# Kernel tuning notes

Hardware: AMD Instinct MI355X
Metric: run time of the kernel (lower is better)

## Reference

```python
import jax, jax.numpy as jnp
import numpy as np

B, T, D = 8, 2048, 1024
GAMMA = 0.96875


def setup_inputs() -> dict:
    key = jax.random.key(0)
    ks = jax.random.split(key, 7)
    sD = 1.0 / np.sqrt(D)
    sT = 1.0 / np.sqrt(T)
    return {
        "x": jax.random.normal(ks[0], (B, T, D), dtype=jnp.float32),
        "Wq": jax.random.normal(ks[1], (D, D), dtype=jnp.float32) * sD,
        "Wk": jax.random.normal(ks[2], (D, D), dtype=jnp.float32) * sD,
        "Wv": jax.random.normal(ks[3], (D, D), dtype=jnp.float32) * sD,
        "W_ih": jax.random.normal(ks[4], (T, T), dtype=jnp.float32) * sT,
        "W_hh": jax.random.normal(ks[5], (T, T), dtype=jnp.float32) * sT,
        "b_ih": jax.random.normal(ks[6], (T,), dtype=jnp.float32) * sT,
    }


def reference(x, Wq, Wk, Wv, W_ih, W_hh, b_ih):
    # x: [B, T, D]; QKV projections (Linear with no bias: x @ W^T)
    Q = jnp.einsum("btd,ed->bte", x, Wq)
    K = jnp.einsum("btd,ed->bte", x, Wk)
    V = jnp.einsum("btd,ed->bte", x, Wv)

    # retention state injected as hidden bias of the tanh-RNN: [B, T]
    bias = jnp.sum(K * V, axis=-1)

    gamma = jnp.full((T,), GAMMA, dtype=x.dtype)
    u = gamma @ W_ih.T + b_ih  # input contribution, identical every step: [T]

    def step(h, b_t):
        h_new = jnp.tanh(u + h @ W_hh.T + b_t)
        return h_new, h_new

    h0 = jnp.zeros((T,), dtype=x.dtype)
    _, S = jax.lax.scan(step, h0, bias)  # scan over the B rows -> S: [B, T]

    # vmap(mul)(S, Q^T)^T  ==  out[b,t,d] = S[b,t] * Q[b,t,d]
    return S[:, :, None] * Q
```

## Files before the change

### kernel.cpp

```cpp
#include <hip/hip_runtime.h>
#include <stdint.h>

#define T_DIM 2048
#define D_DIM 1024
#define B_DIM 8
#define M_TOK (B_DIM * T_DIM)
#define GAMMA_C 0.96875f

typedef float f32x4 __attribute__((ext_vector_type(4)));
typedef float f32x16 __attribute__((ext_vector_type(16)));
typedef float fl4 __attribute__((ext_vector_type(4)));
typedef __bf16 bf16x8 __attribute__((ext_vector_type(8)));
typedef unsigned short us8 __attribute__((ext_vector_type(8)));
typedef unsigned short us4 __attribute__((ext_vector_type(4)));

__device__ __forceinline__ unsigned short f32_bf16_rne(float f) {
  uint32_t u = __builtin_bit_cast(uint32_t, f);
  return (unsigned short)((u + 0x7FFFu + ((u >> 16) & 1u)) >> 16);
}
__device__ __forceinline__ float bf16_f32(unsigned short h) {
  uint32_t u = ((uint32_t)h) << 16;
  return __builtin_bit_cast(float, u);
}

__device__ __forceinline__ int swz_row(int r) {
  return ((r >> 1) & 3) ^ ((r >> 3) & 3);
}

__device__ __forceinline__ void gload16(const void* g, void* l) {
  __builtin_amdgcn_global_load_lds(
      reinterpret_cast<const __attribute__((address_space(1))) uint32_t*>(
          reinterpret_cast<uintptr_t>(g)),
      reinterpret_cast<__attribute__((address_space(3))) uint32_t*>(
          reinterpret_cast<uintptr_t>(l)),
      16, 0, 0);
}

__device__ __forceinline__ bf16x8 ldfrag(const unsigned short* p) {
  us8 u = *reinterpret_cast<const us8*>(p);
  return __builtin_bit_cast(bf16x8, u);
}

#define VMW(n) asm volatile("s_waitcnt vmcnt(" #n ")" ::: "memory")
#define BAR    __builtin_amdgcn_s_barrier()

__global__ __launch_bounds__(256) void k_split(const float* __restrict__ in, int n8,
                                               unsigned short* __restrict__ hi,
                                               unsigned short* __restrict__ lo) {
  int stride = gridDim.x * blockDim.x;
  for (int i = blockIdx.x * blockDim.x + threadIdx.x; i < n8; i += stride) {
    fl4 v0 = ((const fl4*)in)[i * 2];
    fl4 v1 = ((const fl4*)in)[i * 2 + 1];
    us8 h, l;
#pragma unroll
    for (int j = 0; j < 4; ++j) {
      unsigned short hb = f32_bf16_rne(v0[j]);
      h[j] = hb;
      l[j] = f32_bf16_rne(v0[j] - bf16_f32(hb));
      unsigned short hb1 = f32_bf16_rne(v1[j]);
      h[j + 4] = hb1;
      l[j + 4] = f32_bf16_rne(v1[j] - bf16_f32(hb1));
    }
    ((us8*)hi)[i] = h;
    ((us8*)lo)[i] = l;
  }
}

__global__ __launch_bounds__(256) void k_split_hi(const float* __restrict__ in, int n8,
                                                  unsigned short* __restrict__ hi) {
  int stride = gridDim.x * blockDim.x;
  for (int i = blockIdx.x * blockDim.x + threadIdx.x; i < n8; i += stride) {
    fl4 v0 = ((const fl4*)in)[i * 2];
    fl4 v1 = ((const fl4*)in)[i * 2 + 1];
    us8 h;
#pragma unroll
    for (int j = 0; j < 4; ++j) {
      h[j] = f32_bf16_rne(v0[j]);
      h[j + 4] = f32_bf16_rne(v1[j]);
    }
    ((us8*)hi)[i] = h;
  }
}

__global__ __launch_bounds__(256) void k_split_T(const float* __restrict__ in,
                                                 unsigned short* __restrict__ th,
                                                 unsigned short* __restrict__ tl) {
  __shared__ float tile[64][69];
  int be = blockIdx.x >> 4, bd = blockIdx.x & 15;
  int e0 = be * 64, d0 = bd * 64;
  int r = threadIdx.x >> 4;
  int c = (threadIdx.x & 15) * 4;
#pragma unroll
  for (int it = 0; it < 4; ++it) {
    int rr = r + it * 16;
    fl4 v = *(const fl4*)(in + (size_t)(e0 + rr) * D_DIM + d0 + c);
#pragma unroll
    for (int j = 0; j < 4; ++j) tile[rr][c + j] = v[j];
  }
  __syncthreads();
#pragma unroll
  for (int it = 0; it < 4; ++it) {
    int dr = r + it * 16;
    us4 h, l;
#pragma unroll
    for (int j = 0; j < 4; ++j) {
      float f = tile[c + j][dr];
      h[j] = f32_bf16_rne(f);
      l[j] = f32_bf16_rne(f - bf16_f32(h[j]));
    }
    *(us4*)(th + (size_t)(d0 + dr) * D_DIM + e0 + c) = h;
    *(us4*)(tl + (size_t)(d0 + dr) * D_DIM + e0 + c) = l;
  }
}

__global__ __launch_bounds__(256) void k_u(const float* __restrict__ Wih,
                                           const float* __restrict__ bih,
                                           float* __restrict__ u) {
  int wave = threadIdx.x >> 6, lane = threadIdx.x & 63;
  int t = blockIdx.x * 4 + wave;
  const fl4* row = (const fl4*)(Wih + (size_t)t * T_DIM);
  float s = 0.f;
#pragma unroll
  for (int i = 0; i < 8; ++i) {
    fl4 v = row[lane + i * 64];
    s += v[0] + v[1] + v[2] + v[3];
  }
#pragma unroll
  for (int m = 32; m >= 1; m >>= 1) s += __shfl_xor(s, m, 64);
  if (lane == 0) u[t] = GAMMA_C * s + bih[t];
}

__global__ __launch_bounds__(256) void k_step_bf(const unsigned short* __restrict__ Whh_b,
                                                 const float* __restrict__ hprev,
                                                 const float* __restrict__ u,
                                                 const float* __restrict__ biasrow,
                                                 float* __restrict__ hout) {
  int wave = threadIdx.x >> 6, lane = threadIdx.x & 63;
  int t = blockIdx.x * 4 + wave;
  const unsigned short* row = Whh_b + (size_t)t * T_DIM;
  float s = 0.f;
#pragma unroll
  for (int i = 0; i < 4; ++i) {
    us8 w = *(const us8*)(row + i * 512 + lane * 8);
    fl4 h0 = *(const fl4*)(hprev + i * 512 + lane * 8);
    fl4 h1 = *(const fl4*)(hprev + i * 512 + lane * 8 + 4);
    s += bf16_f32(w[0]) * h0[0] + bf16_f32(w[1]) * h0[1] +
         bf16_f32(w[2]) * h0[2] + bf16_f32(w[3]) * h0[3] +
         bf16_f32(w[4]) * h1[0] + bf16_f32(w[5]) * h1[1] +
         bf16_f32(w[6]) * h1[2] + bf16_f32(w[7]) * h1[3];
  }
#pragma unroll
  for (int m = 32; m >= 1; m >>= 1) s += __shfl_xor(s, m, 64);
  if (lane == 0) hout[t] = tanhf(u[t] + s + biasrow[t]);
}

__global__ __launch_bounds__(256) void k_ht(
    const unsigned short* __restrict__ ah, const unsigned short* __restrict__ al,
    const unsigned short* __restrict__ bh, const unsigned short* __restrict__ bl,
    float* __restrict__ Hf) {
  __shared__ unsigned short sAh[2][64 * 32], sAl[2][64 * 32];
  __shared__ unsigned short sBh[2][64 * 32], sBl[2][64 * 32];
  const int tid = threadIdx.x;
  const int wave = tid >> 6, lane = tid & 63;
  const int wm = wave >> 1, wn = wave & 1;
  const int m0 = (blockIdx.x >> 4) * 64, n0 = (blockIdx.x & 15) * 64;
  const int hi32 = lane >> 5;

  const int srow = tid >> 2;
  const int csrc = (tid & 3) ^ swz_row(srow);
  const size_t ga = (size_t)(m0 + srow) * D_DIM + csrc * 8;
  const size_t gb = (size_t)(n0 + srow) * D_DIM + csrc * 8;
  const int ldst = tid * 8;

  f32x16 acc = {};
  const int l31 = lane & 31;
  const int sw = swz_row(l31);
  const int ar = wm * 32 + l31;
  const int br = wn * 32 + l31;
  int aoff[2], boff[2];
#pragma unroll
  for (int kh = 0; kh < 2; ++kh) {
    aoff[kh] = ar * 32 + (((kh * 2 + hi32) ^ sw) * 8);
    boff[kh] = br * 32 + (((kh * 2 + hi32) ^ sw) * 8);
  }

  auto stage = [&](int t, int buf) {
    const size_t ko = (size_t)t * 32;
    gload16(ah + ga + ko, &sAh[buf][ldst]);
    gload16(al + ga + ko, &sAl[buf][ldst]);
    gload16(bh + gb + ko, &sBh[buf][ldst]);
    gload16(bl + gb + ko, &sBl[buf][ldst]);
  };

  stage(0, 0);
  stage(1, 1);
  for (int kt = 0; kt < 32; ++kt) {
    const int cur = kt & 1;
    if (kt < 31) { VMW(4); } else { VMW(0); }
    BAR;
#pragma unroll
    for (int kh = 0; kh < 2; ++kh) {
      bf16x8 fah = ldfrag(&sAh[cur][aoff[kh]]);
      bf16x8 fal = ldfrag(&sAl[cur][aoff[kh]]);
      bf16x8 fbh = ldfrag(&sBh[cur][boff[kh]]);
      bf16x8 fbl = ldfrag(&sBl[cur][boff[kh]]);
      acc = __builtin_amdgcn_mfma_f32_32x32x16_bf16(fah, fbh, acc, 0, 0, 0);
      acc = __builtin_amdgcn_mfma_f32_32x32x16_bf16(fah, fbl, acc, 0, 0, 0);
      acc = __builtin_amdgcn_mfma_f32_32x32x16_bf16(fal, fbh, acc, 0, 0, 0);
    }
    BAR;
    if (kt + 2 <= 31) stage(kt + 2, cur);
  }
#pragma unroll
  for (int r = 0; r < 16; ++r) {
    int row = m0 + wm * 32 + (r & 3) + 8 * (r >> 2) + 4 * hi32;
    int col = n0 + wn * 32 + l31;
    Hf[(size_t)row * D_DIM + col] = acc[r];
  }
}

__global__ __launch_bounds__(256) void k_nprime(const float* __restrict__ Hf,
                                                unsigned short* __restrict__ mh,
                                                unsigned short* __restrict__ ml) {
  __shared__ float t2[64][65];
  const int ti = blockIdx.x >> 4;
  const int tj = blockIdx.x & 15;
  const int r0 = ti * 64, c0 = tj * 64;
  const int a = threadIdx.x >> 2;
  const int b4 = (threadIdx.x & 3) * 16;
  if (tj < ti) {
#pragma unroll
    for (int j = 0; j < 16; ++j) {
      size_t ad = (size_t)(r0 + a) * D_DIM + c0 + b4 + j;
      mh[ad] = 0;
      ml[ad] = 0;
    }
    return;
  }
#pragma unroll
  for (int j = 0; j < 16; j += 4) {
    fl4 v = *(const fl4*)(Hf + (size_t)(c0 + a) * D_DIM + r0 + b4 + j);
#pragma unroll
    for (int q = 0; q < 4; ++q) t2[a][b4 + j + q] = v[q];
  }
  __syncthreads();
#pragma unroll
  for (int j = 0; j < 16; ++j) {
    int dp = r0 + a;
    int dd = c0 + b4 + j;
    float v = 0.f;
    if (dd > dp)       v = Hf[(size_t)dp * D_DIM + dd] + t2[b4 + j][a];
    else if (dd == dp) v = Hf[(size_t)dp * D_DIM + dd];
    unsigned short hb = f32_bf16_rne(v);
    unsigned short lb = f32_bf16_rne(v - bf16_f32(hb));
    size_t ad = (size_t)dp * D_DIM + dd;
    mh[ad] = hb;
    ml[ad] = lb;
  }
}

__global__ __launch_bounds__(256, 4) void k_y_bias(
    const unsigned short* __restrict__ xh, const unsigned short* __restrict__ xl,
    const unsigned short* __restrict__ bh, const unsigned short* __restrict__ bl,
    float* __restrict__ bias) {
  __shared__ unsigned short sAh[2][128 * 16], sAl[2][128 * 16];
  __shared__ unsigned short sBh[2][128 * 16], sBl[2][128 * 16];
  const int tid = threadIdx.x;
  const int wave = tid >> 6, lane = tid & 63;
  const int wm = wave >> 1, wn = wave & 1;
  const int xcd = blockIdx.x & 7, seq = blockIdx.x >> 3;
  const int mb = xcd * 16 + (seq >> 2);
  const int np = seq & 3;
  const int m0 = mb * 128;
  const int hi32 = lane >> 5;
  const int l31 = lane & 31;

  const int srow = tid >> 1;
  const int cch = tid & 1;
  const size_t gA = (size_t)(m0 + srow) * D_DIM + cch * 8;
  const int ldst = tid * 8;

  int aoff[2], boff[2];
#pragma unroll
  for (int mi = 0; mi < 2; ++mi)
    aoff[mi] = (wm * 64 + mi * 32 + l31) * 16 + hi32 * 8;
#pragma unroll
  for (int ni = 0; ni < 2; ++ni)
    boff[ni] = (wn * 64 + ni * 32 + l31) * 16 + hi32 * 8;

  auto phase = [&](int nb) {
    const int n0 = nb * 128;
    const int k0 = nb * 8;
    const int ke = 64;
    const size_t gB = (size_t)(n0 + srow) * D_DIM + cch * 8;

    auto stage = [&](int t, int buf) {
      const size_t ko = (size_t)t * 16;
      gload16(xh + gA + ko, &sAh[buf][ldst]);
      gload16(xl + gA + ko, &sAl[buf][ldst]);
      gload16(bh + gB + ko, &sBh[buf][ldst]);
      gload16(bl + gB + ko, &sBl[buf][ldst]);
    };

    f32x16 acc[2][2] = {};
    stage(k0, 0);
    stage(k0 + 1, 1);
    for (int kt = k0; kt < ke; ++kt) {
      const int cur = (kt - k0) & 1;
      if (kt < ke - 1) { VMW(4); } else { VMW(0); }
      BAR;
      {
        bf16x8 fah[2], fal[2], fbh_[2], fbl_[2];
#pragma unroll
        for (int mi = 0; mi < 2; ++mi) {
          fah[mi] = ldfrag(&sAh[cur][aoff[mi]]);
          fal[mi] = ldfrag(&sAl[cur][aoff[mi]]);
        }
#pragma unroll
        for (int ni = 0; ni < 2; ++ni) {
          fbh_[ni] = ldfrag(&sBh[cur][boff[ni]]);
          fbl_[ni] = ldfrag(&sBl[cur][boff[ni]]);
        }
        __builtin_amdgcn_s_setprio(1);
#pragma unroll
        for (int mi = 0; mi < 2; ++mi)
#pragma unroll
          for (int ni = 0; ni < 2; ++ni) {
            acc[mi][ni] = __builtin_amdgcn_mfma_f32_32x32x16_bf16(fah[mi], fbh_[ni], acc[mi][ni], 0, 0, 0);
            acc[mi][ni] = __builtin_amdgcn_mfma_f32_32x32x16_bf16(fah[mi], fbl_[ni], acc[mi][ni], 0, 0, 0);
            acc[mi][ni] = __builtin_amdgcn_mfma_f32_32x32x16_bf16(fal[mi], fbh_[ni], acc[mi][ni], 0, 0, 0);
          }
        __builtin_amdgcn_s_setprio(0);
      }
      BAR;
      if (kt + 2 < ke) stage(kt + 2, cur);
    }

#pragma unroll
    for (int mi = 0; mi < 2; ++mi)
#pragma unroll
      for (int r = 0; r < 16; ++r) {
        int row = m0 + wm * 64 + mi * 32 + (r & 3) + 8 * (r >> 2) + 4 * hi32;
        size_t ix = (size_t)row * D_DIM + n0 + wn * 64 + l31;
        float xv0 = bf16_f32(xh[ix]) + bf16_f32(xl[ix]);
        float xv1 = bf16_f32(xh[ix + 32]) + bf16_f32(xl[ix + 32]);
        float p = xv0 * acc[mi][0][r] + xv1 * acc[mi][1][r];
        p += __shfl_xor(p, 1, 64);
        p += __shfl_xor(p, 2, 64);
        p += __shfl_xor(p, 4, 64);
        p += __shfl_xor(p, 8, 64);
        p += __shfl_xor(p, 16, 64);
        if (l31 == 0) atomicAdd(&bias[row], p);
      }
  };

  phase(np);
  phase(7 - np);
}

__global__ __launch_bounds__(256, 4) void k_q_out(
    const unsigned short* __restrict__ xh,
    const unsigned short* __restrict__ qh_,
    const float* __restrict__ S, float* __restrict__ out) {
  __shared__ unsigned short sA[2][128 * 32];
  __shared__ unsigned short sB[2][128 * 32];
  const int tid = threadIdx.x;
  const int wave = tid >> 6, lane = tid & 63;
  const int wm = wave >> 1, wn = wave & 1;
  int sw0 = (blockIdx.x & 7) * 128 + (blockIdx.x >> 3);
  const int mb = sw0 >> 3, nb = sw0 & 7;
  const int m0 = mb * 128, n0 = nb * 128;
  const int hi32 = lane >> 5;
  const int l31 = lane & 31;

  const int srow0 = tid >> 2, srow1 = srow0 + 64;
  const int csrc0 = (tid & 3) ^ swz_row(srow0);
  const int csrc1 = (tid & 3) ^ swz_row(srow1);
  const size_t gaA0 = (size_t)(m0 + srow0) * D_DIM + csrc0 * 8;
  const size_t gaA1 = (size_t)(m0 + srow1) * D_DIM + csrc1 * 8;
  const size_t gaB0 = (size_t)(n0 + srow0) * D_DIM + csrc0 * 8;
  const size_t gaB1 = (size_t)(n0 + srow1) * D_DIM + csrc1 * 8;
  const int ldst0 = tid * 8, ldst1 = (tid + 256) * 8;

  f32x16 acc[2][2] = {};
  int aoff[2][2], boff[2][2];
#pragma unroll
  for (int mi = 0; mi < 2; ++mi) {
    int r = wm * 64 + mi * 32 + l31;
    int sw = swz_row(r);
#pragma unroll
    for (int kh = 0; kh < 2; ++kh)
      aoff[mi][kh] = r * 32 + (((kh * 2 + hi32) ^ sw) * 8);
  }
#pragma unroll
  for (int ni = 0; ni < 2; ++ni) {
    int r = wn * 64 + ni * 32 + l31;
    int sw = swz_row(r);
#pragma unroll
    for (int kh = 0; kh < 2; ++kh)
      boff[ni][kh] = r * 32 + (((kh * 2 + hi32) ^ sw) * 8);
  }

  auto stage = [&](int t, int buf) {
    const size_t ko = (size_t)t * 32;
    gload16(xh + gaA0 + ko, &sA[buf][ldst0]);
    gload16(xh + gaA1 + ko, &sA[buf][ldst1]);
    gload16(qh_ + gaB0 + ko, &sB[buf][ldst0]);
    gload16(qh_ + gaB1 + ko, &sB[buf][ldst1]);
  };

  stage(0, 0);
  stage(1, 1);
  for (int kt = 0; kt < 32; ++kt) {
    const int cur = kt & 1;
    if (kt < 31) { VMW(4); } else { VMW(0); }
    BAR;
#pragma unroll
    for (int kh = 0; kh < 2; ++kh) {
      bf16x8 fa[2], fb[2];
#pragma unroll
      for (int mi = 0; mi < 2; ++mi) fa[mi] = ldfrag(&sA[cur][aoff[mi][kh]]);
#pragma unroll
      for (int ni = 0; ni < 2; ++ni) fb[ni] = ldfrag(&sB[cur][boff[ni][kh]]);
      __builtin_amdgcn_s_setprio(1);
#pragma unroll
      for (int mi = 0; mi < 2; ++mi)
#pragma unroll
        for (int ni = 0; ni < 2; ++ni)
          acc[mi][ni] = __builtin_amdgcn_mfma_f32_32x32x16_bf16(fa[mi], fb[ni], acc[mi][ni], 0, 0, 0);
      __builtin_amdgcn_s_setprio(0);
    }
    BAR;
    if (kt + 2 <= 31) stage(kt + 2, cur);
  }

#pragma unroll
  for (int mi = 0; mi < 2; ++mi)
#pragma unroll
    for (int r = 0; r < 16; ++r) {
      int row = m0 + wm * 64 + mi * 32 + (r & 3) + 8 * (r >> 2) + 4 * hi32;
      float sc = S[row];
      float* orow = out + (size_t)row * D_DIM + n0 + wn * 64 + l31;
      orow[0] = sc * acc[mi][0][r];
      orow[32] = sc * acc[mi][1][r];
    }
}

extern "C" void kernel_launch(void* const* d_in, const int* in_sizes, int n_in,
                              void* d_out, int out_size, void* d_ws, size_t ws_size,
                              hipStream_t stream) {
  const float* x   = (const float*)d_in[0];
  const float* Wq  = (const float*)d_in[1];
  const float* Wk  = (const float*)d_in[2];
  const float* Wv  = (const float*)d_in[3];
  const float* Wih = (const float*)d_in[4];
  const float* Whh = (const float*)d_in[5];
  const float* bih = (const float*)d_in[6];
  float* out = (float*)d_out;

  char* ws = (char*)d_ws;
  size_t off = 0;
  auto alloc = [&](size_t bytes) -> char* {
    char* p = ws + off;
    off += (bytes + 255) & ~(size_t)255;
    return p;
  };
  unsigned short* xh   = (unsigned short*)alloc((size_t)M_TOK * D_DIM * 2);
  unsigned short* xl   = (unsigned short*)alloc((size_t)M_TOK * D_DIM * 2);
  unsigned short* wqh  = (unsigned short*)alloc((size_t)D_DIM * D_DIM * 2);
  unsigned short* wkth = (unsigned short*)alloc((size_t)D_DIM * D_DIM * 2);
  unsigned short* wktl = (unsigned short*)alloc((size_t)D_DIM * D_DIM * 2);
  unsigned short* wvth = (unsigned short*)alloc((size_t)D_DIM * D_DIM * 2);
  unsigned short* wvtl = (unsigned short*)alloc((size_t)D_DIM * D_DIM * 2);
  unsigned short* mph  = (unsigned short*)alloc((size_t)D_DIM * D_DIM * 2);
  unsigned short* mpl  = (unsigned short*)alloc((size_t)D_DIM * D_DIM * 2);
  float* Hf   = (float*)alloc((size_t)D_DIM * D_DIM * 4);
  float* bias = (float*)alloc((size_t)M_TOK * 4);
  float* Sbuf = (float*)alloc((size_t)M_TOK * 4);
  float* ubuf = (float*)alloc((size_t)T_DIM * 4);
  float* zbuf = (float*)alloc((size_t)T_DIM * 4);
  unsigned short* whhb = wkth;
  (void)ws_size; (void)in_sizes; (void)n_in; (void)out_size;

  k_split<<<2048, 256, 0, stream>>>(x, M_TOK * D_DIM / 8, xh, xl);
  k_split_hi<<<512, 256, 0, stream>>>(Wq, D_DIM * D_DIM / 8, wqh);
  k_split_T<<<256, 256, 0, stream>>>(Wk, wkth, wktl);
  k_split_T<<<256, 256, 0, stream>>>(Wv, wvth, wvtl);

  hipMemsetAsync(bias, 0, (size_t)M_TOK * 4, stream);
  hipMemsetAsync(zbuf, 0, (size_t)T_DIM * 4, stream);

  k_u<<<T_DIM / 4, 256, 0, stream>>>(Wih, bih, ubuf);

  k_ht<<<256, 256, 0, stream>>>(wvth, wvtl, wkth, wktl, Hf);

  k_nprime<<<256, 256, 0, stream>>>(Hf, mph, mpl);

  k_split_hi<<<1024, 256, 0, stream>>>(Whh, T_DIM * T_DIM / 8, whhb);

  k_y_bias<<<512, 256, 0, stream>>>(xh, xl, mph, mpl, bias);

  for (int b = 0; b < B_DIM; ++b) {
    const float* hp = (b == 0) ? zbuf : (Sbuf + (size_t)(b - 1) * T_DIM);
    k_step_bf<<<T_DIM / 4, 256, 0, stream>>>(whhb, hp, ubuf, bias + (size_t)b * T_DIM,
                                             Sbuf + (size_t)b * T_DIM);
  }

  k_q_out<<<1024, 256, 0, stream>>>(xh, wqh, Sbuf, out);
}
```

Measured before the change: 290.4 us.

## Restructure bias GEMM: 512 threads, K=32 tiles, triple-buffered swizzled LDS

The bias-GEMM kernel now runs 512 threads per block in an 8-wave 2x4 layout, so each wave computes a 64x32 subtile. It stages K=32 slices instead of 16, with XOR-swizzled LDS rows to avoid bank conflicts. A three-buffer ring replaces the double buffer, which lets the next stage load be issued right after the barrier and drops the second barrier per iteration. The aim is to cut barrier and LDS-conflict overhead and overlap loads with MFMA work. The cost is higher LDS use (96KB per block), which may lower occupancy, and it depends on a swz_row helper defined elsewhere.

```diff
diff --git a/kernel.cpp b/kernel.cpp
--- a/kernel.cpp
+++ b/kernel.cpp
@@ -259,15 +259,15 @@
   }
 }
 
-__global__ __launch_bounds__(256, 4) void k_y_bias(
+__global__ __launch_bounds__(512, 2) void k_y_bias(
     const unsigned short* __restrict__ xh, const unsigned short* __restrict__ xl,
     const unsigned short* __restrict__ bh, const unsigned short* __restrict__ bl,
     float* __restrict__ bias) {
-  __shared__ unsigned short sAh[2][128 * 16], sAl[2][128 * 16];
-  __shared__ unsigned short sBh[2][128 * 16], sBl[2][128 * 16];
+  __shared__ unsigned short sAh[3][128 * 32], sAl[3][128 * 32];
+  __shared__ unsigned short sBh[3][128 * 32], sBl[3][128 * 32];
   const int tid = threadIdx.x;
   const int wave = tid >> 6, lane = tid & 63;
-  const int wm = wave >> 1, wn = wave & 1;
+  const int wm = wave >> 2, wn = wave & 3;
   const int xcd = blockIdx.x & 7, seq = blockIdx.x >> 3;
   const int mb = xcd * 16 + (seq >> 2);
   const int np = seq & 3;
@@ -275,65 +275,71 @@
   const int hi32 = lane >> 5;
   const int l31 = lane & 31;
 
-  const int srow = tid >> 1;
-  const int cch = tid & 1;
-  const size_t gA = (size_t)(m0 + srow) * D_DIM + cch * 8;
+  const int srow = tid >> 2;
+  const int csrc = (tid & 3) ^ swz_row(srow);
+  const size_t gA = (size_t)(m0 + srow) * D_DIM + csrc * 8;
   const int ldst = tid * 8;
 
-  int aoff[2], boff[2];
-#pragma unroll
-  for (int mi = 0; mi < 2; ++mi)
-    aoff[mi] = (wm * 64 + mi * 32 + l31) * 16 + hi32 * 8;
-#pragma unroll
-  for (int ni = 0; ni < 2; ++ni)
-    boff[ni] = (wn * 64 + ni * 32 + l31) * 16 + hi32 * 8;
+  int aoff[2][2], boff[2];
+#pragma unroll
+  for (int mi = 0; mi < 2; ++mi) {
+    int r = wm * 64 + mi * 32 + l31;
+    int sw = swz_row(r);
+#pragma unroll
+    for (int kh = 0; kh < 2; ++kh)
+      aoff[mi][kh] = r * 32 + (((kh * 2 + hi32) ^ sw) * 8);
+  }
+  {
+    int r = wn * 32 + l31;
+    int sw = swz_row(r);
+#pragma unroll
+    for (int kh = 0; kh < 2; ++kh)
+      boff[kh] = r * 32 + (((kh * 2 + hi32) ^ sw) * 8);
+  }
 
   auto phase = [&](int nb) {
     const int n0 = nb * 128;
-    const int k0 = nb * 8;
-    const int ke = 64;
-    const size_t gB = (size_t)(n0 + srow) * D_DIM + cch * 8;
+    const int k0 = nb * 4, ke = 32;
+    const size_t gB = (size_t)(n0 + srow) * D_DIM + csrc * 8;
 
     auto stage = [&](int t, int buf) {
-      const size_t ko = (size_t)t * 16;
+      const size_t ko = (size_t)t * 32;
       gload16(xh + gA + ko, &sAh[buf][ldst]);
       gload16(xl + gA + ko, &sAl[buf][ldst]);
       gload16(bh + gB + ko, &sBh[buf][ldst]);
       gload16(bl + gB + ko, &sBl[buf][ldst]);
     };
 
-    f32x16 acc[2][2] = {};
+    f32x16 acc[2] = {};
+    BAR;
     stage(k0, 0);
     stage(k0 + 1, 1);
+    int cur = 0;
     for (int kt = k0; kt < ke; ++kt) {
-      const int cur = (kt - k0) & 1;
       if (kt < ke - 1) { VMW(4); } else { VMW(0); }
       BAR;
-      {
-        bf16x8 fah[2], fal[2], fbh_[2], fbl_[2];
+      int nx = cur + 2; if (nx >= 3) nx -= 3;
+      if (kt + 2 < ke) stage(kt + 2, nx);
+#pragma unroll
+      for (int kh = 0; kh < 2; ++kh) {
+        bf16x8 fah[2], fal[2];
 #pragma unroll
         for (int mi = 0; mi < 2; ++mi) {
-          fah[mi] = ldfrag(&sAh[cur][aoff[mi]]);
-          fal[mi] = ldfrag(&sAl[cur][aoff[mi]]);
+          fah[mi] = ldfrag(&sAh[cur][aoff[mi][kh]]);
+          fal[mi] = ldfrag(&sAl[cur][aoff[mi][kh]]);
         }
-#pragma unroll
-        for (int ni = 0; ni < 2; ++ni) {
-          fbh_[ni] = ldfrag(&sBh[cur][boff[ni]]);
-          fbl_[ni] = ldfrag(&sBl[cur][boff[ni]]);
+        bf16x8 fbh = ldfrag(&sBh[cur][boff[kh]]);
+        bf16x8 fbl = ldfrag(&sBl[cur][boff[kh]]);
+        __builtin_amdgcn_s_setprio(1);
+#pragma unroll
+        for (int mi = 0; mi < 2; ++mi) {
+          acc[mi] = __builtin_amdgcn_mfma_f32_32x32x16_bf16(fah[mi], fbh, acc[mi], 0, 0, 0);
+          acc[mi] = __builtin_amdgcn_mfma_f32_32x32x16_bf16(fah[mi], fbl, acc[mi], 0, 0, 0);
+          acc[mi] = __builtin_amdgcn_mfma_f32_32x32x16_bf16(fal[mi], fbh, acc[mi], 0, 0, 0);
         }
-        __builtin_amdgcn_s_setprio(1);
-#pragma unroll
-        for (int mi = 0; mi < 2; ++mi)
-#pragma unroll
-          for (int ni = 0; ni < 2; ++ni) {
-            acc[mi][ni] = __builtin_amdgcn_mfma_f32_32x32x16_bf16(fah[mi], fbh_[ni], acc[mi][ni], 0, 0, 0);
-            acc[mi][ni] = __builtin_amdgcn_mfma_f32_32x32x16_bf16(fah[mi], fbl_[ni], acc[mi][ni], 0, 0, 0);
-            acc[mi][ni] = __builtin_amdgcn_mfma_f32_32x32x16_bf16(fal[mi], fbh_[ni], acc[mi][ni], 0, 0, 0);
-          }
         __builtin_amdgcn_s_setprio(0);
       }
-      BAR;
-      if (kt + 2 < ke) stage(kt + 2, cur);
+      cur = cur + 1; if (cur >= 3) cur -= 3;
     }
 
 #pragma unroll
@@ -341,10 +347,9 @@
 #pragma unroll
       for (int r = 0; r < 16; ++r) {
         int row = m0 + wm * 64 + mi * 32 + (r & 3) + 8 * (r >> 2) + 4 * hi32;
-        size_t ix = (size_t)row * D_DIM + n0 + wn * 64 + l31;
-        float xv0 = bf16_f32(xh[ix]) + bf16_f32(xl[ix]);
-        float xv1 = bf16_f32(xh[ix + 32]) + bf16_f32(xl[ix + 32]);
-        float p = xv0 * acc[mi][0][r] + xv1 * acc[mi][1][r];
+        size_t ix = (size_t)row * D_DIM + n0 + wn * 32 + l31;
+        float xv = bf16_f32(xh[ix]) + bf16_f32(xl[ix]);
+        float p = xv * acc[mi][r];
         p += __shfl_xor(p, 1, 64);
         p += __shfl_xor(p, 2, 64);
         p += __shfl_xor(p, 4, 64);
@@ -498,7 +503,7 @@
 
   k_split_hi<<<1024, 256, 0, stream>>>(Whh, T_DIM * T_DIM / 8, whhb);
 
-  k_y_bias<<<512, 256, 0, stream>>>(xh, xl, mph, mpl, bias);
+  k_y_bias<<<512, 512, 0, stream>>>(xh, xl, mph, mpl, bias);
 
   for (int b = 0; b < B_DIM; ++b) {
     const float* hp = (b == 0) ? zbuf : (Sbuf + (size_t)(b - 1) * T_DIM);
```

Result: faster. 267.9 us (-7.7%).
